# Optimization experiments

Measured on AMD Instinct MI355X. Metric: run time of the kernel, lower is better.

The kernel has to match this reference:

```python
import jax, jax.numpy as jnp
import numpy as np

EPS = 1e-5  # torch BatchNorm1d default eps
N0, N, ORIG, F, K, H, NC = 16, 96, 92, 64, 41, 128, 3


def _bn(x, g, b, axes):
    # training-mode batchnorm: biased batch stats over `axes`, per-channel affine
    m = jnp.mean(x, axis=axes, keepdims=True)
    v = jnp.mean((x - m) ** 2, axis=axes, keepdims=True)
    return (x - m) / jnp.sqrt(v + EPS) * g + b


def setup_inputs() -> dict:
    key = jax.random.key(0)
    ks = jax.random.split(key, 16)
    s = 0.05
    return {
        "atom_fea": jax.random.normal(ks[0], (N0, N, ORIG), jnp.float32),
        "nbr_fea": jax.random.normal(ks[1], (N0, N, N, K), jnp.float32),
        "adj": jax.random.randint(ks[2], (N0, N, N), 0, 2, jnp.int64),
        "emb_W": jax.random.normal(ks[3], (ORIG, F), jnp.float32) * s,
        "emb_b": jnp.zeros((F,), jnp.float32),
        "conv_W": jax.random.normal(ks[4], (NC, 2 * F + K, 2 * F), jnp.float32) * s,
        "conv_b": jnp.zeros((NC, 2 * F), jnp.float32),
        "bn1_g": jnp.ones((NC, 2 * F), jnp.float32),
        "bn1_b": jnp.zeros((NC, 2 * F), jnp.float32),
        "bn2_g": jnp.ones((NC, F), jnp.float32),
        "bn2_b": jnp.zeros((NC, F), jnp.float32),
        "fc_W": jax.random.normal(ks[5], (F, H), jnp.float32) * s,
        "fc_b": jnp.zeros((H,), jnp.float32),
        "out_W": jax.random.normal(ks[6], (H, 1), jnp.float32) * s,
        "out_b": jnp.zeros((1,), jnp.float32),
    }


def reference(atom_fea, nbr_fea, adj, emb_W, emb_b, conv_W, conv_b,
              bn1_g, bn1_b, bn2_g, bn2_b, fc_W, fc_b, out_W, out_b):
    fea = atom_fea @ emb_W + emb_b                       # (N0, N, F)
    adjf = adj.astype(fea.dtype)[..., None]              # (N0, N, N, 1)
    for i in range(NC):
        # NOTE: faithful to source - both FEA and masked term broadcast atom j's
        # own features along the neighbor axis (unsqueeze(2) in torch code).
        FEA = jnp.broadcast_to(fea[:, :, None, :], (N0, N, N, F))
        total = jnp.concatenate([FEA, adjf * FEA, nbr_fea], axis=3)   # (N0,N,N,2F+K)
        gated = total @ conv_W[i] + conv_b[i]                         # (N0,N,N,2F)
        gated = _bn(gated, bn1_g[i], bn1_b[i], (0, 1, 2))
        filt, core = jnp.split(gated, 2, axis=3)
        summed = jnp.sum(jax.nn.sigmoid(filt) * jax.nn.softplus(core), axis=2)  # (N0,N,F)
        summed = _bn(summed, bn2_g[i], bn2_b[i], (0, 1))
        fea = jax.nn.softplus(fea + summed)
    crys = jnp.mean(fea, axis=1)                                      # (N0, F)
    crys = jax.nn.softplus(jax.nn.softplus(crys) @ fc_W + fc_b)       # (N0, H)
    return crys @ out_W + out_b                                       # (N0, 1)
```

## Files before the change

kernel.cpp:

```cpp
#include <hip/hip_runtime.h>
#include <math.h>

#define N0c   16
#define NAt   96
#define ORIG  92
#define Fc    64
#define Kc    41
#define Hc    128
#define NCc   3
#define C2    128
#define EPSBN 1e-5f
#define JG    4
#define JPW   (NAt / JG)
#define NREP  32
#define SRL_STRIDE 12288
#define AROW  72
#define WFRAG 16384
#define INV1  (1.f / (float)(N0c * NAt * NAt))
#define INV2  (1.f / (float)(N0c * NAt))

typedef __attribute__((ext_vector_type(8))) short short8_t;
typedef __attribute__((ext_vector_type(4))) float f32x4;

__device__ __forceinline__ float sp_(float x){
    return fmaxf(x, 0.f) + __logf(1.f + __expf(-fabsf(x)));
}
__device__ __forceinline__ float sgm_(float x){
    return 1.f / (1.f + __expf(-x));
}
__device__ __forceinline__ unsigned short bfhi(float x){
    union { float f; unsigned u; } v; v.f = x;
    unsigned r = v.u + 0x7fff + ((v.u >> 16) & 1);
    return (unsigned short)(r >> 16);
}
__device__ __forceinline__ float bf2f(unsigned short h){
    union { float f; unsigned u; } v; v.u = ((unsigned)h) << 16; return v.f;
}

__global__ __launch_bounds__(256) void k_pre(const float* __restrict__ nbr,
                                             const int*   __restrict__ adj,
                                             float* __restrict__ ST,
                                             float* __restrict__ cntf){
    int r    = blockIdx.x;
    int lane = threadIdx.x & 63;
    int jg   = __builtin_amdgcn_readfirstlane(threadIdx.x >> 6);
    __shared__ float rS[JG][Kc], rT[JG][Kc], rc[JG];
    float S = 0.f, T = 0.f, cn = 0.f;
    int j0 = jg * JPW;
    for (int j = j0; j < j0 + JPW; ++j){
        float a = (float)adj[r * NAt + j];
        float v = (lane < Kc) ? nbr[((size_t)r * NAt + j) * Kc + lane] : 0.f;
        S += v; T += a * v; cn += a;
    }
    if (lane < Kc){ rS[jg][lane] = S; rT[jg][lane] = T; }
    if (lane == 0) rc[jg] = cn;
    __syncthreads();
    int t = threadIdx.x;
    if (t < Kc){
        ST[r * (2 * Kc) + t]      = rS[0][t] + rS[1][t] + rS[2][t] + rS[3][t];
        ST[r * (2 * Kc) + Kc + t] = rT[0][t] + rT[1][t] + rT[2][t] + rT[3][t];
    }
    if (t == 0) cntf[r] = rc[0] + rc[1] + rc[2] + rc[3];
}

__global__ __launch_bounds__(128) void k_gram(const float* __restrict__ nbr,
                                              const int*   __restrict__ adj,
                                              float* __restrict__ pG,
                                              float* __restrict__ ST,
                                              float* __restrict__ cntf,
                                              float* __restrict__ G,
                                              int rpb, int doST){
    int blk = blockIdx.x;
    int t   = threadIdx.x;
    int k   = (t % 21) * 2;
    int lb  = (t / 21) * 7;
    __shared__ float L[NAt * Kc];
    __shared__ float AJf[NAt];
    if (blk == 0){
        for (int i = t; i < Kc * Kc; i += 128) G[i] = 0.f;
    }
    float a0[7] = {0,0,0,0,0,0,0}, a1[7] = {0,0,0,0,0,0,0};
    for (int rr = 0; rr < rpb; ++rr){
        int r = blk * rpb + rr;
        __syncthreads();
        for (int i = t; i < NAt * Kc; i += 128)
            L[i] = nbr[(size_t)r * NAt * Kc + i];
        if (t < NAt) AJf[t] = (float)adj[r * NAt + t];
        __syncthreads();
        if (doST && t < Kc){
            float S = 0.f, T = 0.f;
            for (int j = 0; j < NAt; ++j){
                float v = L[j * Kc + t];
                S += v; T += AJf[j] * v;
            }
            ST[r * (2 * Kc) + t]      = S;
            ST[r * (2 * Kc) + Kc + t] = T;
        }
        if (doST && t == Kc){
            float cn = 0.f;
            for (int j = 0; j < NAt; ++j) cn += AJf[j];
            cntf[r] = cn;
        }
        if (t < 126){
            for (int j = 0; j < NAt; ++j){
                float vk0 = L[j * Kc + k];
                float vk1 = (k + 1 < Kc) ? L[j * Kc + k + 1] : 0.f;
                #pragma unroll
                for (int m = 0; m < 7; ++m){
                    if (lb + m < Kc){
                        float lv = L[j * Kc + lb + m];
                        a0[m] += vk0 * lv;
                        a1[m] += vk1 * lv;
                    }
                }
            }
        }
    }
    if (t < 126){
        float* dst = pG + (size_t)blk * (Kc * Kc);
        #pragma unroll
        for (int m = 0; m < 7; ++m){
            if (lb + m < Kc){
                dst[k * Kc + lb + m] = a0[m];
                if (k + 1 < Kc) dst[(k + 1) * Kc + lb + m] = a1[m];
            }
        }
    }
}

__global__ __launch_bounds__(64) void k_gred(const float* __restrict__ pG,
                                             float* __restrict__ G){
    int i  = (blockIdx.x % 27) * 64 + threadIdx.x;
    int b0 = (blockIdx.x / 27) * 96;
    if (i < Kc * Kc){
        float s = 0.f;
        #pragma unroll 4
        for (int b = b0; b < b0 + 96; ++b) s += pG[(size_t)b * (Kc * Kc) + i];
        atomicAdd(&G[i], s);
    }
}

__global__ __launch_bounds__(256) void k_prep(const float* __restrict__ G,
                                              const float* __restrict__ convW,
                                              float* __restrict__ W3T,
                                              unsigned short* __restrict__ W3F,
                                              float* __restrict__ q3){
    int l   = blockIdx.x;
    int tid = threadIdx.x;
    const float* Wl = convW + (size_t)l * 169 * C2;
    __shared__ float GL[Kc * Kc];
    for (int i = tid; i < Kc * Kc; i += 256) GL[i] = G[i];
    __syncthreads();
    for (int it = 0; it < 8; ++it){
        int idx  = tid + it * 256;
        int lane = idx & 63;
        int fid  = idx >> 6;
        int h    = fid & 1;
        int ks   = (fid >> 1) & 1;
        int nt   = fid >> 2;
        int n    = nt * 16 + (lane & 15);
        unsigned short* dst = W3F + (size_t)l * WFRAG + fid * 512 + lane * 8;
        #pragma unroll
        for (int i = 0; i < 8; ++i){
            int kk = ks * 32 + (lane >> 4) * 8 + i;
            float w = (kk < Kc) ? Wl[(C2 + kk) * C2 + n] : 0.f;
            unsigned short hi = bfhi(w);
            dst[i] = h ? bfhi(w - bf2f(hi)) : hi;
        }
    }
    if (tid < C2){
        int c = tid;
        float* dstT = W3T + ((size_t)l * C2 + c) * 44;
        float w3[Kc];
        #pragma unroll
        for (int kk = 0; kk < Kc; ++kk){
            w3[kk] = Wl[(C2 + kk) * C2 + c];
            dstT[kk] = w3[kk];
        }
        dstT[41] = 0.f; dstT[42] = 0.f; dstT[43] = 0.f;
        float q = 0.f;
        for (int kk = 0; kk < Kc; ++kk){
            float gw = 0.f;
            #pragma unroll
            for (int m = 0; m < Kc; ++m) gw += GL[kk * Kc + m] * w3[m];
            q += w3[kk] * gw;
        }
        q3[l * C2 + c] = q;
    }
}

__global__ __launch_bounds__(256)
void k_front(float* __restrict__ fea,
             const float* __restrict__ atom,
             const float* __restrict__ embW,
             const float* __restrict__ embB,
             const float* __restrict__ Wl,
             const float* __restrict__ bl,
             const float* __restrict__ W3Tl,
             const float* __restrict__ ST,
             const float* __restrict__ cntf,
             float* __restrict__ p1,
             float* __restrict__ p2,
             float* __restrict__ sum1R,
             float* __restrict__ sq1R,
             const float* __restrict__ summed,
             const float* __restrict__ sum2Rp,
             const float* __restrict__ sq2Rp,
             const float* __restrict__ g2p,
             const float* __restrict__ b2p,
             int upd){
    int r    = blockIdx.x;
    int tid  = threadIdx.x;
    int c    = tid & 127;
    int half = __builtin_amdgcn_readfirstlane(tid >> 7);
    __shared__ float F[Fc];
    __shared__ float A2L[Fc], B2L[Fc];
    __shared__ float P1h[C2], P2h[C2], TTs[C2];

    if (upd){
        if (tid < Fc){
            float s = 0.f, q = 0.f;
            for (int rr = 0; rr < NREP; ++rr){
                s += sum2Rp[rr * Fc + tid];
                q += sq2Rp[rr * Fc + tid];
            }
            float m = s * INV2;
            float v = q * INV2 - m * m;
            float A = g2p[tid] * rsqrtf(v + EPSBN);
            A2L[tid] = A;
            B2L[tid] = b2p[tid] - m * A;
        }
        __syncthreads();
        if (tid < Fc){
            float nv = sp_(fea[r * Fc + tid] + summed[r * Fc + tid] * A2L[tid] + B2L[tid]);
            F[tid] = nv;
            fea[r * Fc + tid] = nv;
        }
        __syncthreads();
    } else {
        if (tid < Fc){
            const float* ar = atom + r * ORIG;
            float acc = embB[tid];
            #pragma unroll 4
            for (int o = 0; o < ORIG; ++o) acc += ar[o] * embW[o * Fc + tid];
            F[tid] = acc;
            fea[r * Fc + tid] = acc;
        }
        __syncthreads();
    }

    float a1p = 0.f, a2p = 0.f;
    int f0 = half * 32;
    #pragma unroll 8
    for (int f = f0; f < f0 + 32; ++f){
        float fv = F[f];
        a1p += fv * Wl[f * C2 + c];
        a2p += fv * Wl[(Fc + f) * C2 + c];
    }
    const float* wt = W3Tl + c * 44;
    const float* Sr = ST + r * (2 * Kc) + half * Kc;
    float dot = 0.f;
    #pragma unroll
    for (int k = 0; k < 40; k += 4){
        float4 wv = *(const float4*)(wt + k);
        dot += Sr[k] * wv.x + Sr[k + 1] * wv.y + Sr[k + 2] * wv.z + Sr[k + 3] * wv.w;
    }
    dot += Sr[40] * wt[40];

    if (half == 1){ P1h[c] = a1p; P2h[c] = a2p; TTs[c] = dot; }
    __syncthreads();
    if (half == 0){
        float a1 = a1p + P1h[c] + bl[c];
        float a2 = a2p + P2h[c];
        float u  = dot;
        float tt = TTs[c];
        p1[r * C2 + c] = a1;
        p2[r * C2 + c] = a2;
        float cn = cntf[r];
        float s1 = (float)NAt * a1 + cn * a2 + u;
        float q1 = (float)NAt * a1 * a1 + cn * a2 * a2
                 + 2.f * cn * a1 * a2 + 2.f * a1 * u + 2.f * a2 * tt;
        int slot = blockIdx.x & (NREP - 1);
        atomicAdd(&sum1R[slot * C2 + c], s1);
        atomicAdd(&sq1R[slot * C2 + c], q1);
    }
}

__global__ __launch_bounds__(512)
void k_apply(const float* __restrict__ nbr,
             const int*   __restrict__ adj,
             const unsigned short* __restrict__ W3Fl,
             const float* __restrict__ p1,
             const float* __restrict__ p2,
             const float* __restrict__ sum1R,
             const float* __restrict__ sq1R,
             const float* __restrict__ qv,
             const float* __restrict__ g1,
             const float* __restrict__ b1,
             float* __restrict__ summed,
             float* __restrict__ sum2R,
             float* __restrict__ sq2R){
    int r    = blockIdx.x;
    int tid  = threadIdx.x;
    int lane = tid & 63;
    int w    = __builtin_amdgcn_readfirstlane(tid >> 6);
    int ntF  = w & 3;
    int mh   = w >> 2;

    __shared__ unsigned short sAH[NAt * AROW];
    __shared__ unsigned short sAL[NAt * AROW];
    __shared__ float AJ[NAt];
    __shared__ float PL1[C2], PL2[C2], A1L[C2], B1L[C2];
    __shared__ float TpW[8][16];

    short8_t BH[2][2], BL[2][2];
    #pragma unroll
    for (int ni = 0; ni < 2; ++ni){
        int nt = ntF + ni * 4;
        #pragma unroll
        for (int ks = 0; ks < 2; ++ks){
            int fidH = (nt * 2 + ks) * 2;
            BH[ni][ks] = *(const short8_t*)(W3Fl + fidH * 512 + lane * 8);
            BL[ni][ks] = *(const short8_t*)(W3Fl + (fidH + 1) * 512 + lane * 8);
        }
    }

    const float* nb = nbr + (size_t)r * (NAt * Kc);
    for (int idx = tid; idx < NAt * Kc; idx += 512){
        int j = idx / Kc, k = idx - j * Kc;
        float x = nb[idx];
        unsigned short hi = bfhi(x);
        sAH[j * AROW + k] = hi;
        sAL[j * AROW + k] = bfhi(x - bf2f(hi));
    }
    for (int idx = tid; idx < NAt * 23; idx += 512){
        int j = idx / 23, k = Kc + (idx - j * 23);
        sAH[j * AROW + k] = 0;
        sAL[j * AROW + k] = 0;
    }
    if (tid < C2){
        int c = tid;
        float s = 0.f, q = 0.f;
        for (int rr = 0; rr < NREP; ++rr){ s += sum1R[rr * C2 + c]; q += sq1R[rr * C2 + c]; }
        float m = s * INV1;
        float v = (q + qv[c]) * INV1 - m * m;
        float A = g1[c] * rsqrtf(v + EPSBN);
        A1L[c] = A;
        B1L[c] = b1[c] - m * A;
    } else if (tid < 256){
        PL1[tid - 128] = p1[r * C2 + tid - 128];
    } else if (tid < 384){
        PL2[tid - 256] = p2[r * C2 + tid - 256];
    } else if (tid < 480){
        AJ[tid - 384] = (float)adj[r * NAt + tid - 384];
    }
    __syncthreads();

    f32x4 acc[3][2] = {};
    int q4 = (lane >> 4) * 8;
    #pragma unroll
    for (int mt = 0; mt < 3; ++mt){
        int jrow = (mh * 48 + mt * 16 + (lane & 15)) * AROW;
        short8_t AH0 = *(const short8_t*)(&sAH[jrow + q4]);
        short8_t AH1 = *(const short8_t*)(&sAH[jrow + 32 + q4]);
        short8_t AL0 = *(const short8_t*)(&sAL[jrow + q4]);
        short8_t AL1 = *(const short8_t*)(&sAL[jrow + 32 + q4]);
        #pragma unroll
        for (int ni = 0; ni < 2; ++ni){
            acc[mt][ni] = __builtin_amdgcn_mfma_f32_16x16x32_bf16(AH0, BH[ni][0], acc[mt][ni], 0, 0, 0);
            acc[mt][ni] = __builtin_amdgcn_mfma_f32_16x16x32_bf16(AH0, BL[ni][0], acc[mt][ni], 0, 0, 0);
            acc[mt][ni] = __builtin_amdgcn_mfma_f32_16x16x32_bf16(AL0, BH[ni][0], acc[mt][ni], 0, 0, 0);
            acc[mt][ni] = __builtin_amdgcn_mfma_f32_16x16x32_bf16(AH1, BH[ni][1], acc[mt][ni], 0, 0, 0);
            acc[mt][ni] = __builtin_amdgcn_mfma_f32_16x16x32_bf16(AH1, BL[ni][1], acc[mt][ni], 0, 0, 0);
            acc[mt][ni] = __builtin_amdgcn_mfma_f32_16x16x32_bf16(AL1, BH[ni][1], acc[mt][ni], 0, 0, 0);
        }
    }

    int cF = ntF * 16 + (lane & 15);
    int cC = cF + 64;
    float p1F = PL1[cF], p2F = PL2[cF], A1F = A1L[cF], B1F = B1L[cF];
    float p1C = PL1[cC], p2C = PL2[cC], A1C = A1L[cC], B1C = B1L[cC];
    float tsum = 0.f;
    #pragma unroll
    for (int mt = 0; mt < 3; ++mt){
        #pragma unroll
        for (int rg = 0; rg < 4; ++rg){
            int j = mh * 48 + mt * 16 + (lane >> 4) * 4 + rg;
            float ajf = AJ[j];
            float gf = (p1F + ajf * p2F + acc[mt][0][rg]) * A1F + B1F;
            float gc = (p1C + ajf * p2C + acc[mt][1][rg]) * A1C + B1C;
            tsum += sgm_(gf) * sp_(gc);
        }
    }
    tsum += __shfl_xor(tsum, 16);
    tsum += __shfl_xor(tsum, 32);
    if (lane < 16) TpW[w][lane] = tsum;
    __syncthreads();
    if (tid < Fc){
        int f = tid;
        float s = TpW[f >> 4][f & 15] + TpW[(f >> 4) + 4][f & 15];
        summed[r * Fc + f] = s;
        int slot = blockIdx.x & (NREP - 1);
        atomicAdd(&sum2R[slot * Fc + f], s);
        atomicAdd(&sq2R[slot * Fc + f], s * s);
    }
}

__global__ __launch_bounds__(128) void k_final(const float* __restrict__ fea,
                                               const float* __restrict__ summed,
                                               const float* __restrict__ sum2R,
                                               const float* __restrict__ sq2R,
                                               const float* __restrict__ g2,
                                               const float* __restrict__ b2,
                                               const float* __restrict__ fcW,
                                               const float* __restrict__ fcb,
                                               const float* __restrict__ outW,
                                               const float* __restrict__ outb,
                                               float* __restrict__ out){
    int b = blockIdx.x;
    int t = threadIdx.x;
    __shared__ float spc[Fc];
    __shared__ float red[Hc];
    if (t < Fc){
        float s = 0.f, q = 0.f;
        for (int r = 0; r < NREP; ++r){ s += sum2R[r * Fc + t]; q += sq2R[r * Fc + t]; }
        float m  = s * INV2;
        float v  = q * INV2 - m * m;
        float A2 = g2[t] * rsqrtf(v + EPSBN);
        float B2 = b2[t] - m * A2;
        float acc = 0.f;
        for (int i = 0; i < NAt; ++i){
            int idx = (b * NAt + i) * Fc + t;
            acc += sp_(fea[idx] + summed[idx] * A2 + B2);
        }
        spc[t] = sp_(acc * (1.f / NAt));
    }
    __syncthreads();
    float h = fcb[t];
    #pragma unroll 4
    for (int f = 0; f < Fc; ++f) h += spc[f] * fcW[f * Hc + t];
    h = sp_(h);
    red[t] = h * outW[t];
    __syncthreads();
    for (int off = 64; off > 0; off >>= 1){
        if (t < off) red[t] += red[t + off];
        __syncthreads();
    }
    if (t == 0) out[b] = red[0] + outb[0];
}

extern "C" void kernel_launch(void* const* d_in, const int* in_sizes, int n_in,
                              void* d_out, int out_size, void* d_ws, size_t ws_size,
                              hipStream_t stream){
    const float* atom  = (const float*)d_in[0];
    const float* nbr   = (const float*)d_in[1];
    const int*   adj   = (const int*)  d_in[2];
    const float* embW  = (const float*)d_in[3];
    const float* embB  = (const float*)d_in[4];
    const float* convW = (const float*)d_in[5];
    const float* convB = (const float*)d_in[6];
    const float* bn1g  = (const float*)d_in[7];
    const float* bn1b  = (const float*)d_in[8];
    const float* bn2g  = (const float*)d_in[9];
    const float* bn2b  = (const float*)d_in[10];
    const float* fcW   = (const float*)d_in[11];
    const float* fcb   = (const float*)d_in[12];
    const float* outW  = (const float*)d_in[13];
    const float* outb  = (const float*)d_in[14];
    float* out = (float*)d_out;
    float* ws  = (float*)d_ws;

    const int ROWS = N0c * NAt;
    float* fea    = ws;
    float* p1     = ws + 98304;
    float* p2     = ws + 294912;
    float* summed = ws + 491520;
    float* SRL    = ws + 589824;
    float* ST     = ws + 626688;
    float* cntf   = ws + 752640;
    float* q3     = ws + 754176;
    float* W3T    = ws + 754560;
    unsigned short* W3F = (unsigned short*)(ws + 771456);
    const size_t PERS = 796032;

    size_t ws_f = ws_size / sizeof(float);
    int nblk; float *pG, *G; int compact = 0;
    if (ws_f >= PERS + (size_t)1536 * 1681 + 1681 + 64){
        nblk = 1536; pG = ws + PERS; G = pG + (size_t)nblk * 1681;
    } else if (ws_f >= PERS + (size_t)768 * 1681 + 1681 + 64){
        nblk = 768;  pG = ws + PERS; G = pG + (size_t)nblk * 1681;
    } else if (ws_f >= PERS + (size_t)384 * 1681 + 1681 + 64){
        nblk = 384;  pG = ws + PERS; G = pG + (size_t)nblk * 1681;
    } else {
        nblk = 384;  pG = ws;        G = ws + 650000;  compact = 1;
    }
    int rpb = 1536 / nblk;
    int ph  = nblk / 96;

    k_gram <<<nblk, 128, 0, stream>>>(nbr, adj, pG, ST, cntf, G, rpb,
                                      compact ? 0 : 1);
    k_gred <<<27 * ph, 64, 0, stream>>>(pG, G);
    k_prep <<<NCc, 256, 0, stream>>>(G, convW, W3T, W3F, q3);
    if (compact)
        k_pre <<<ROWS, 256, 0, stream>>>(nbr, adj, ST, cntf);
    hipMemsetAsync(SRL, 0, 3 * SRL_STRIDE * sizeof(float), stream);

    for (int l = 0; l < NCc; ++l){
        const float* Wl   = convW + (size_t)l * 169 * C2;
        const float* bl   = convB + l * C2;
        const float* W3Tl = W3T + (size_t)l * C2 * 44;
        const unsigned short* W3Fl = W3F + (size_t)l * WFRAG;
        float* sum1R = SRL + l * SRL_STRIDE;
        float* sq1R  = sum1R + 4096;
        float* sum2R = sum1R + 8192;
        float* sq2R  = sum1R + 10240;
        const float* sum2Rp = (l > 0) ? SRL + (l - 1) * SRL_STRIDE + 8192 : SRL;
        const float* sq2Rp  = (l > 0) ? SRL + (l - 1) * SRL_STRIDE + 10240 : SRL;
        const float* g2p    = bn2g + (l > 0 ? (l - 1) : 0) * Fc;
        const float* b2p    = bn2b + (l > 0 ? (l - 1) : 0) * Fc;

        k_front <<<ROWS, 256, 0, stream>>>(fea, atom, embW, embB,
                                           Wl, bl, W3Tl, ST, cntf,
                                           p1, p2, sum1R, sq1R,
                                           summed, sum2Rp, sq2Rp, g2p, b2p,
                                           l > 0 ? 1 : 0);
        k_apply <<<ROWS, 512, 0, stream>>>(nbr, adj, W3Fl, p1, p2,
                                           sum1R, sq1R, q3 + l * C2,
                                           bn1g + l * C2, bn1b + l * C2,
                                           summed, sum2R, sq2R);
    }

    k_final<<<N0c, Hc, 0, stream>>>(fea, summed,
                                    SRL + 2 * SRL_STRIDE + 8192,
                                    SRL + 2 * SRL_STRIDE + 10240,
                                    bn2g + 2 * Fc, bn2b + 2 * Fc,
                                    fcW, fcb, outW, outb, out);
}
```

Before: 288.7 us.

## Parallelize weight-prep kernel across 96 blocks with per-wave quadratic forms

The weight-preparation kernel previously ran on only three blocks, with one thread per output channel doing a serial 41x41 quadratic form. It now launches 32 blocks per layer with five waves each. Four waves each compute one channel's quadratic form, one lane per row, finishing with a wavefront shuffle reduction. The fifth wave writes one bf16 split-fragment group. This removes a long serial tail on a tiny grid, at the cost of more blocks each reloading the 41x41 Gram matrix into shared memory.

```diff
diff --git a/kernel.cpp b/kernel.cpp
--- a/kernel.cpp
+++ b/kernel.cpp
@@ -140,52 +140,59 @@
     }
 }
 
-__global__ __launch_bounds__(256) void k_prep(const float* __restrict__ G,
+__global__ __launch_bounds__(320) void k_prep(const float* __restrict__ G,
                                               const float* __restrict__ convW,
                                               float* __restrict__ W3T,
                                               unsigned short* __restrict__ W3F,
                                               float* __restrict__ q3){
-    int l   = blockIdx.x;
-    int tid = threadIdx.x;
+    int bi   = blockIdx.x;
+    int l    = bi >> 5;
+    int g    = bi & 31;
+    int tid  = threadIdx.x;
+    int lane = tid & 63;
+    int w    = __builtin_amdgcn_readfirstlane(tid >> 6);
     const float* Wl = convW + (size_t)l * 169 * C2;
     __shared__ float GL[Kc * Kc];
-    for (int i = tid; i < Kc * Kc; i += 256) GL[i] = G[i];
-    __syncthreads();
-    for (int it = 0; it < 8; ++it){
-        int idx  = tid + it * 256;
-        int lane = idx & 63;
-        int fid  = idx >> 6;
-        int h    = fid & 1;
-        int ks   = (fid >> 1) & 1;
-        int nt   = fid >> 2;
-        int n    = nt * 16 + (lane & 15);
-        unsigned short* dst = W3F + (size_t)l * WFRAG + fid * 512 + lane * 8;
+    __shared__ float w3s[4][Kc];
+    for (int i = tid; i < Kc * Kc; i += 320) GL[i] = G[i];
+
+    int   c  = g * 4 + (w & 3);
+    float w3 = 0.f;
+    if (w < 4){
+        w3 = (lane < Kc) ? Wl[(C2 + lane) * C2 + c] : 0.f;
+        if (lane < 44)
+            W3T[((size_t)l * C2 + c) * 44 + lane] = (lane < Kc) ? w3 : 0.f;
+        if (lane < Kc) w3s[w][lane] = w3;
+    }
+    __syncthreads();
+
+    if (w == 4){
+        int h  = g & 1;
+        int ks = (g >> 1) & 1;
+        int nt = g >> 2;
+        int n  = nt * 16 + (lane & 15);
+        unsigned short* dst = W3F + (size_t)l * WFRAG + g * 512 + lane * 8;
         #pragma unroll
         for (int i = 0; i < 8; ++i){
             int kk = ks * 32 + (lane >> 4) * 8 + i;
-            float w = (kk < Kc) ? Wl[(C2 + kk) * C2 + n] : 0.f;
-            unsigned short hi = bfhi(w);
-            dst[i] = h ? bfhi(w - bf2f(hi)) : hi;
-        }
-    }
-    if (tid < C2){
-        int c = tid;
-        float* dstT = W3T + ((size_t)l * C2 + c) * 44;
-        float w3[Kc];
-        #pragma unroll
-        for (int kk = 0; kk < Kc; ++kk){
-            w3[kk] = Wl[(C2 + kk) * C2 + c];
-            dstT[kk] = w3[kk];
-        }
-        dstT[41] = 0.f; dstT[42] = 0.f; dstT[43] = 0.f;
-        float q = 0.f;
-        for (int kk = 0; kk < Kc; ++kk){
-            float gw = 0.f;
+            float x = (kk < Kc) ? Wl[(C2 + kk) * C2 + n] : 0.f;
+            unsigned short hi = bfhi(x);
+            dst[i] = h ? bfhi(x - bf2f(hi)) : hi;
+        }
+    } else {
+        float gw = 0.f;
+        if (lane < Kc){
             #pragma unroll
-            for (int m = 0; m < Kc; ++m) gw += GL[kk * Kc + m] * w3[m];
-            q += w3[kk] * gw;
-        }
-        q3[l * C2 + c] = q;
+            for (int m = 0; m < Kc; ++m) gw += GL[lane * Kc + m] * w3s[w][m];
+        }
+        float part = (lane < Kc) ? w3 * gw : 0.f;
+        part += __shfl_xor(part, 1);
+        part += __shfl_xor(part, 2);
+        part += __shfl_xor(part, 4);
+        part += __shfl_xor(part, 8);
+        part += __shfl_xor(part, 16);
+        part += __shfl_xor(part, 32);
+        if (lane == 0) q3[l * C2 + c] = part;
     }
 }
 
@@ -500,7 +507,7 @@
     k_gram <<<nblk, 128, 0, stream>>>(nbr, adj, pG, ST, cntf, G, rpb,
                                       compact ? 0 : 1);
     k_gred <<<27 * ph, 64, 0, stream>>>(pG, G);
-    k_prep <<<NCc, 256, 0, stream>>>(G, convW, W3T, W3F, q3);
+    k_prep <<<NCc * 32, 320, 0, stream>>>(G, convW, W3T, W3F, q3);
     if (compact)
         k_pre <<<ROWS, 256, 0, stream>>>(nbr, adj, ST, cntf);
     hipMemsetAsync(SRL, 0, 3 * SRL_STRIDE * sizeof(float), stream);
```

New measurement: 263.0 us. -8.9%, faster.
